# Optimization experiments

Measured on AMD Instinct MI355X. Metric: run time of the kernel, lower is better.

## Reference

```python
import jax, jax.numpy as jnp
import numpy as np

N_NODES = 50000
N_EDGES = 800000
F_IN = 128


def _sage_conv(x, src, dst, W_l, b_l, W_r, n_nodes):
    # PyG SAGEConv (mean aggr, normalize=False, root_weight=True):
    #   out_i = W_l @ mean_{j in N(i)} x_j + b_l + W_r @ x_i
    msg = x[src]  # [E, F] gather
    agg = jax.ops.segment_sum(msg, dst, num_segments=n_nodes)  # [N, F]
    cnt = jax.ops.segment_sum(jnp.ones((src.shape[0],), x.dtype), dst,
                              num_segments=n_nodes)  # [N]
    mean = agg / jnp.maximum(cnt, 1.0)[:, None]
    return mean @ W_l.T + b_l + x @ W_r.T


def setup_inputs() -> dict:
    key = jax.random.key(0)
    ks = jax.random.split(key, 16)
    inp = {}
    inp["x"] = jax.random.normal(ks[0], (N_NODES, F_IN), dtype=jnp.float32)
    inp["edge_index"] = jax.random.randint(ks[1], (2, N_EDGES), 0, N_NODES, dtype=jnp.int64)
    inp["reg_id"] = jax.random.randint(ks[2], (N_NODES,), 0, 22, dtype=jnp.int64)
    inp["dep_id"] = jax.random.randint(ks[3], (N_NODES,), 0, 96, dtype=jnp.int64)
    # learned parameters (kaiming-ish small random)
    inp["W_feat"] = jax.random.normal(ks[4], (32, F_IN), dtype=jnp.float32) * (1.0 / np.sqrt(F_IN))
    inp["b_feat"] = jnp.zeros((32,), dtype=jnp.float32)
    inp["reg_emb"] = jax.random.normal(ks[5], (22, 16), dtype=jnp.float32)
    inp["dep_emb"] = jax.random.normal(ks[6], (96, 16), dtype=jnp.float32)
    inp["W1_l"] = jax.random.normal(ks[7], (16, 64), dtype=jnp.float32) * 0.125
    inp["b1_l"] = jnp.zeros((16,), dtype=jnp.float32)
    inp["W1_r"] = jax.random.normal(ks[8], (16, 64), dtype=jnp.float32) * 0.125
    inp["W2_l"] = jax.random.normal(ks[9], (32, 16), dtype=jnp.float32) * 0.25
    inp["b2_l"] = jnp.zeros((32,), dtype=jnp.float32)
    inp["W2_r"] = jax.random.normal(ks[10], (32, 16), dtype=jnp.float32) * 0.25
    inp["W_lin"] = jax.random.normal(ks[11], (1, 32), dtype=jnp.float32) * 0.1767767
    inp["b_lin"] = jnp.zeros((1,), dtype=jnp.float32)
    return inp


def reference(x, edge_index, reg_id, dep_id, W_feat, b_feat, reg_emb, dep_emb,
              W1_l, b1_l, W1_r, W2_l, b2_l, W2_r, W_lin, b_lin):
    src, dst = edge_index[0], edge_index[1]
    reg_fm = reg_emb[reg_id]            # [N, 16]
    dep_fm = dep_emb[dep_id]            # [N, 16]
    h = x @ W_feat.T + b_feat           # [N, 32]
    h = jnp.concatenate([h, reg_fm, dep_fm], axis=1)  # [N, 64]
    h = jax.nn.relu(_sage_conv(h, src, dst, W1_l, b1_l, W1_r, N_NODES))  # [N, 16]
    h = jax.nn.relu(_sage_conv(h, src, dst, W2_l, b2_l, W2_r, N_NODES))  # [N, 32]
    return h @ W_lin.T + b_lin          # [N, 1]
```

## Files before the change

kernel.cpp:

```cpp
#include <hip/hip_runtime.h>

#define N_NODES 50000
#define N_EDGES 800000
#define HB 128
#define CHUNK (N_EDGES / HB)
#define CNTW ((N_NODES + 3) / 4)
#define NODE1_BLOCKS ((N_NODES + 63) / 64)
#define SCAN_BLK 256
#define SCAN_NBLK ((N_NODES + SCAN_BLK - 1) / SCAN_BLK)

__device__ __forceinline__ unsigned short f2bf(float f) {
    unsigned int b = __float_as_uint(f);
    b += 0x7fffu + ((b >> 16) & 1u);
    return (unsigned short)(b >> 16);
}

__global__ __launch_bounds__(256) void node1_hist_kernel(
    const float* __restrict__ x, const int* __restrict__ reg_id,
    const int* __restrict__ dep_id,
    const float* __restrict__ W_feat, const float* __restrict__ b_feat,
    const float* __restrict__ reg_emb, const float* __restrict__ dep_emb,
    const float* __restrict__ W1_l, const float* __restrict__ W1_r,
    const int* __restrict__ ei,
    unsigned short* __restrict__ p1bf, float* __restrict__ r1,
    unsigned int* __restrict__ part, unsigned char* __restrict__ lrank)
{
    __shared__ union U {
        struct N1 { float sx[64 * 132]; float sh[64 * 68]; } n1;
        unsigned int cnt[CNTW];
    } u;
    const int tid = threadIdx.x;

    if (blockIdx.x >= NODE1_BLOCKS) {
        const int g  = blockIdx.x - NODE1_BLOCKS;
        const int e0 = g * CHUNK;
        for (int i = tid; i < CNTW; i += 256) u.cnt[i] = 0u;
        __syncthreads();
        for (int i = tid; i < CHUNK; i += 256) {
            int d = ei[N_EDGES + e0 + i];
            unsigned sh_ = (unsigned)(d & 3) * 8u;
            unsigned old = atomicAdd(&u.cnt[d >> 2], 1u << sh_);
            lrank[e0 + i] = (unsigned char)((old >> sh_) & 0xffu);
        }
        __syncthreads();
        for (int i = tid; i < CNTW; i += 256)
            part[g * CNTW + i] = u.cnt[i];
        return;
    }

    const int node0 = blockIdx.x * 64;
    for (int i = tid; i < 64 * 32; i += 256) {
        int row = i >> 5, c4 = i & 31;
        float4 v = make_float4(0.f, 0.f, 0.f, 0.f);
        int n = node0 + row;
        if (n < N_NODES) v = *(const float4*)&x[n * 128 + c4 * 4];
        *(float4*)&u.n1.sx[row * 132 + c4 * 4] = v;
    }
    for (int i = tid; i < 64 * 16; i += 256) {
        int r = i >> 4, f = i & 15;
        int n = node0 + r;
        if (n < N_NODES) {
            u.n1.sh[r * 68 + 32 + f] = reg_emb[reg_id[n] * 16 + f];
            u.n1.sh[r * 68 + 48 + f] = dep_emb[dep_id[n] * 16 + f];
        }
    }
    __syncthreads();

    const int nl = tid & 63;
    const int j0 = __builtin_amdgcn_readfirstlane((tid >> 6) * 8);

    {
        float acc[8];
        #pragma unroll
        for (int jj = 0; jj < 8; ++jj) acc[jj] = b_feat[j0 + jj];
        #pragma unroll 4
        for (int k = 0; k < 128; k += 4) {
            float4 xv = *(const float4*)&u.n1.sx[nl * 132 + k];
            #pragma unroll
            for (int jj = 0; jj < 8; ++jj) {
                const float* wr = &W_feat[(j0 + jj) * 128 + k];
                acc[jj] += xv.x * wr[0] + xv.y * wr[1] + xv.z * wr[2] + xv.w * wr[3];
            }
        }
        #pragma unroll
        for (int jj = 0; jj < 8; ++jj) u.n1.sh[nl * 68 + j0 + jj] = acc[jj];
    }
    __syncthreads();

    {
        const float* Wbase = (j0 < 16) ? (W1_l + j0 * 64) : (W1_r + (j0 - 16) * 64);
        float acc[8];
        #pragma unroll
        for (int jj = 0; jj < 8; ++jj) acc[jj] = 0.f;
        #pragma unroll 4
        for (int k = 0; k < 64; k += 4) {
            float4 hv = *(const float4*)&u.n1.sh[nl * 68 + k];
            #pragma unroll
            for (int jj = 0; jj < 8; ++jj) {
                const float* wr = &Wbase[jj * 64 + k];
                acc[jj] += hv.x * wr[0] + hv.y * wr[1] + hv.z * wr[2] + hv.w * wr[3];
            }
        }
        int n = node0 + nl;
        if (n < N_NODES) {
            if (j0 < 16) {
                uint4 q;
                q.x = ((unsigned)f2bf(acc[1]) << 16) | f2bf(acc[0]);
                q.y = ((unsigned)f2bf(acc[3]) << 16) | f2bf(acc[2]);
                q.z = ((unsigned)f2bf(acc[5]) << 16) | f2bf(acc[4]);
                q.w = ((unsigned)f2bf(acc[7]) << 16) | f2bf(acc[6]);
                *(uint4*)&p1bf[n * 16 + j0] = q;
            } else {
                float* outp = r1 + n * 16 + (j0 - 16);
                *(float4*)outp       = make_float4(acc[0], acc[1], acc[2], acc[3]);
                *(float4*)(outp + 4) = make_float4(acc[4], acc[5], acc[6], acc[7]);
            }
        }
    }
}

__global__ __launch_bounds__(256) void bpscan_kernel(
    const unsigned int* __restrict__ part, unsigned char* __restrict__ bp,
    int* __restrict__ rowp1, int* __restrict__ parts)
{
    __shared__ int buf[2][256];
    int t = threadIdx.x;
    int n = blockIdx.x * 256 + t;
    int deg = 0;
    if (n < N_NODES) {
        int w = n >> 2;
        unsigned sh_ = (unsigned)(n & 3) * 8u;
        unsigned int loc[HB / 4];
        int s = 0;
        #pragma unroll
        for (int q = 0; q < HB / 4; ++q) {
            unsigned int wdat = 0;
            #pragma unroll
            for (int j = 0; j < 4; ++j) {
                wdat |= (unsigned)(s & 0xff) << (8 * j);
                s += (int)((part[(q * 4 + j) * CNTW + w] >> sh_) & 0xffu);
            }
            loc[q] = wdat;
        }
        deg = s;
        uint4* dst = (uint4*)&bp[(size_t)n * HB];
        const uint4* src = (const uint4*)loc;
        #pragma unroll
        for (int q = 0; q < HB / 16; ++q) dst[q] = src[q];
    }
    buf[0][t] = deg;
    __syncthreads();
    int cur = 0;
    for (int off = 1; off < 256; off <<= 1) {
        int nv = buf[cur][t] + ((t >= off) ? buf[cur][t - off] : 0);
        buf[cur ^ 1][t] = nv;
        cur ^= 1;
        __syncthreads();
    }
    int incl = buf[cur][t];
    if (n < N_NODES) rowp1[n] = incl - deg;
    if (t == 255) parts[blockIdx.x] = incl;
}

__global__ __launch_bounds__(256) void scanparts_kernel(
    const int* __restrict__ parts, int* __restrict__ poff)
{
    __shared__ int buf[2][256];
    int t = threadIdx.x;
    int pv = (t < SCAN_NBLK) ? parts[t] : 0;
    buf[0][t] = pv;
    __syncthreads();
    int cur = 0;
    for (int off = 1; off < 256; off <<= 1) {
        int nv = buf[cur][t] + ((t >= off) ? buf[cur][t - off] : 0);
        buf[cur ^ 1][t] = nv;
        cur ^= 1;
        __syncthreads();
    }
    if (t < SCAN_NBLK) poff[t] = buf[cur][t] - pv;
}

__global__ __launch_bounds__(256) void fill_kernel(
    const int* __restrict__ ei, const unsigned char* __restrict__ lrank,
    const int* __restrict__ rowp1, const int* __restrict__ poff,
    const unsigned char* __restrict__ bp, int* __restrict__ csrc)
{
    int t4 = (blockIdx.x * 256 + threadIdx.x) * 4;
    if (t4 >= N_EDGES) return;
    uint4 sv = *(const uint4*)&ei[t4];
    uint4 dv = *(const uint4*)&ei[N_EDGES + t4];
    unsigned lr4 = *(const unsigned*)&lrank[t4];

    #pragma unroll
    for (int j = 0; j < 4; ++j) {
        int d = (j == 0) ? (int)dv.x : (j == 1) ? (int)dv.y
              : (j == 2) ? (int)dv.z : (int)dv.w;
        int s = (j == 0) ? (int)sv.x : (j == 1) ? (int)sv.y
              : (j == 2) ? (int)sv.z : (int)sv.w;
        int g = (t4 + j) / CHUNK;
        int pos = rowp1[d] + poff[d >> 8] + (int)bp[(size_t)d * HB + g]
                + (int)((lr4 >> (8 * j)) & 0xffu);
        csrc[pos] = s;
    }
}

__global__ __launch_bounds__(256) void gather1_kernel(
    const int* __restrict__ rowp1, const int* __restrict__ poff,
    const int* __restrict__ csrc,
    const unsigned short* __restrict__ p1bf, const float* __restrict__ r1,
    const float* __restrict__ b1_l, unsigned short* __restrict__ h1bf)
{
    int n = (blockIdx.x * 256 + threadIdx.x) >> 6;
    int lane = threadIdx.x & 63;
    int slot = lane >> 2, f4 = lane & 3;
    int start = rowp1[n] + poff[n >> 8];
    int end = (n + 1 < N_NODES) ? rowp1[n + 1] + poff[(n + 1) >> 8] : N_EDGES;

    float4 acc = make_float4(0.f, 0.f, 0.f, 0.f);
    for (int eb = start; eb < end; eb += 16) {
        int e = eb + slot;
        if (e < end) {
            uint2 v = *(const uint2*)&p1bf[csrc[e] * 16 + f4 * 4];
            acc.x += __uint_as_float(v.x << 16);
            acc.y += __uint_as_float(v.x & 0xffff0000u);
            acc.z += __uint_as_float(v.y << 16);
            acc.w += __uint_as_float(v.y & 0xffff0000u);
        }
    }
    #pragma unroll
    for (int off = 4; off <= 32; off <<= 1) {
        acc.x += __shfl_xor(acc.x, off, 64);
        acc.y += __shfl_xor(acc.y, off, 64);
        acc.z += __shfl_xor(acc.z, off, 64);
        acc.w += __shfl_xor(acc.w, off, 64);
    }
    if (slot == 0) {
        float inv = 1.0f / fmaxf((float)(end - start), 1.0f);
        float4 rv = *(const float4*)&r1[n * 16 + f4 * 4];
        float4 bv = *(const float4*)&b1_l[f4 * 4];
        float ox = fmaxf(acc.x * inv + bv.x + rv.x, 0.f);
        float oy = fmaxf(acc.y * inv + bv.y + rv.y, 0.f);
        float oz = fmaxf(acc.z * inv + bv.z + rv.z, 0.f);
        float ow = fmaxf(acc.w * inv + bv.w + rv.w, 0.f);
        uint2 w;
        w.x = ((unsigned)f2bf(oy) << 16) | f2bf(ox);
        w.y = ((unsigned)f2bf(ow) << 16) | f2bf(oz);
        *(uint2*)&h1bf[n * 16 + f4 * 4] = w;
    }
}

__global__ __launch_bounds__(256) void gather2_kernel(
    const int* __restrict__ rowp1, const int* __restrict__ poff,
    const int* __restrict__ csrc, const unsigned short* __restrict__ h1bf,
    const float* __restrict__ W2_l, const float* __restrict__ b2_l,
    const float* __restrict__ W2_r, const float* __restrict__ W_lin,
    const float* __restrict__ b_lin, float* __restrict__ out)
{
    int n = (blockIdx.x * 256 + threadIdx.x) >> 6;
    int lane = threadIdx.x & 63;
    int slot = lane >> 2, f4 = lane & 3;
    int start = rowp1[n] + poff[n >> 8];
    int end = (n + 1 < N_NODES) ? rowp1[n + 1] + poff[(n + 1) >> 8] : N_EDGES;

    float4 acc = make_float4(0.f, 0.f, 0.f, 0.f);
    for (int eb = start; eb < end; eb += 16) {
        int e = eb + slot;
        if (e < end) {
            uint2 v = *(const uint2*)&h1bf[csrc[e] * 16 + f4 * 4];
            acc.x += __uint_as_float(v.x << 16);
            acc.y += __uint_as_float(v.x & 0xffff0000u);
            acc.z += __uint_as_float(v.y << 16);
            acc.w += __uint_as_float(v.y & 0xffff0000u);
        }
    }
    #pragma unroll
    for (int off = 4; off <= 32; off <<= 1) {
        acc.x += __shfl_xor(acc.x, off, 64);
        acc.y += __shfl_xor(acc.y, off, 64);
        acc.z += __shfl_xor(acc.z, off, 64);
        acc.w += __shfl_xor(acc.w, off, 64);
    }
    float inv = 1.0f / fmaxf((float)(end - start), 1.0f);
    float4 m2 = make_float4(acc.x * inv, acc.y * inv, acc.z * inv, acc.w * inv);
    uint2 hv = *(const uint2*)&h1bf[n * 16 + f4 * 4];
    float hn0 = __uint_as_float(hv.x << 16);
    float hn1 = __uint_as_float(hv.x & 0xffff0000u);
    float hn2 = __uint_as_float(hv.y << 16);
    float hn3 = __uint_as_float(hv.y & 0xffff0000u);

    int j0 = slot * 2;
    float4 wl0 = *(const float4*)&W2_l[j0 * 16 + f4 * 4];
    float4 wl1 = *(const float4*)&W2_l[(j0 + 1) * 16 + f4 * 4];
    float4 wr0 = *(const float4*)&W2_r[j0 * 16 + f4 * 4];
    float4 wr1 = *(const float4*)&W2_r[(j0 + 1) * 16 + f4 * 4];

    float pa = m2.x * wl0.x + m2.y * wl0.y + m2.z * wl0.z + m2.w * wl0.w
             + hn0 * wr0.x + hn1 * wr0.y + hn2 * wr0.z + hn3 * wr0.w;
    float pb = m2.x * wl1.x + m2.y * wl1.y + m2.z * wl1.z + m2.w * wl1.w
             + hn0 * wr1.x + hn1 * wr1.y + hn2 * wr1.z + hn3 * wr1.w;
    pa += __shfl_xor(pa, 1, 64); pa += __shfl_xor(pa, 2, 64);
    pb += __shfl_xor(pb, 1, 64); pb += __shfl_xor(pb, 2, 64);

    float h2a = fmaxf(pa + b2_l[j0], 0.f);
    float h2b = fmaxf(pb + b2_l[j0 + 1], 0.f);
    float w = h2a * W_lin[j0] + h2b * W_lin[j0 + 1];
    #pragma unroll
    for (int off = 4; off <= 32; off <<= 1) w += __shfl_xor(w, off, 64);
    if (lane == 0) out[n] = w + b_lin[0];
}

extern "C" void kernel_launch(void* const* d_in, const int* in_sizes, int n_in,
                              void* d_out, int out_size, void* d_ws, size_t ws_size,
                              hipStream_t stream) {
    const float* x       = (const float*)d_in[0];
    const int*   ei      = (const int*)  d_in[1];
    const int*   reg_id  = (const int*)  d_in[2];
    const int*   dep_id  = (const int*)  d_in[3];
    const float* W_feat  = (const float*)d_in[4];
    const float* b_feat  = (const float*)d_in[5];
    const float* reg_emb = (const float*)d_in[6];
    const float* dep_emb = (const float*)d_in[7];
    const float* W1_l    = (const float*)d_in[8];
    const float* b1_l    = (const float*)d_in[9];
    const float* W1_r    = (const float*)d_in[10];
    const float* W2_l    = (const float*)d_in[11];
    const float* b2_l    = (const float*)d_in[12];
    const float* W2_r    = (const float*)d_in[13];
    const float* W_lin   = (const float*)d_in[14];
    const float* b_lin   = (const float*)d_in[15];
    float* out = (float*)d_out;
    float* ws  = (float*)d_ws;

    const int N = N_NODES;
    float* r1 = ws;
    unsigned int* part = (unsigned int*)(ws + 16 * N);
    int* csrc  = (int*)(part + HB * CNTW);
    int* rowp1 = csrc + N_EDGES;
    int* parts = rowp1 + N;
    int* poff  = parts + 256;
    unsigned short* p1bf = (unsigned short*)(poff + 256);
    unsigned short* h1bf = p1bf + 16 * N;
    unsigned char* lrank = (unsigned char*)(h1bf + 16 * N);
    unsigned char* bp    = lrank + N_EDGES;

    node1_hist_kernel<<<NODE1_BLOCKS + HB, 256, 0, stream>>>(
        x, reg_id, dep_id, W_feat, b_feat, reg_emb, dep_emb, W1_l, W1_r,
        ei, p1bf, r1, part, lrank);

    bpscan_kernel<<<SCAN_NBLK, 256, 0, stream>>>(part, bp, rowp1, parts);

    scanparts_kernel<<<1, 256, 0, stream>>>(parts, poff);

    fill_kernel<<<(N_EDGES / 4 + 255) / 256, 256, 0, stream>>>(
        ei, lrank, rowp1, poff, bp, csrc);

    gather1_kernel<<<(N * 64) / 256, 256, 0, stream>>>(
        rowp1, poff, csrc, p1bf, r1, b1_l, h1bf);

    gather2_kernel<<<(N * 64) / 256, 256, 0, stream>>>(
        rowp1, poff, csrc, h1bf, W2_l, b2_l, W2_r, W_lin, b_lin, out);
}
```

Baseline: 104.7 us.

## Fuse bucket scan, partial-sum scan and CSR fill into one kernel with grid barrier

Merges the per-node prefix scan, the single-block scan of block partials, and the CSR fill into one kernel. The last block to finish, found through an atomic counter, scans the partials and sets a flag, and the other blocks spin on that flag before running a grid-strided fill. The control words are reset in the first kernel. This removes two kernel launches and their gaps. In exchange it relies on all 196 blocks being resident at once for the spin-wait, and the fill now runs on fewer threads that each loop over more edges.

```diff
diff --git a/kernel.cpp b/kernel.cpp
--- a/kernel.cpp
+++ b/kernel.cpp
@@ -23,13 +23,19 @@
     const float* __restrict__ W1_l, const float* __restrict__ W1_r,
     const int* __restrict__ ei,
     unsigned short* __restrict__ p1bf, float* __restrict__ r1,
-    unsigned int* __restrict__ part, unsigned char* __restrict__ lrank)
+    unsigned int* __restrict__ part, unsigned char* __restrict__ lrank,
+    int* __restrict__ ctrl)
 {
     __shared__ union U {
         struct N1 { float sx[64 * 132]; float sh[64 * 68]; } n1;
         unsigned int cnt[CNTW];
     } u;
     const int tid = threadIdx.x;
+
+    if (blockIdx.x == 0 && tid < 2) {
+        __hip_atomic_store(&ctrl[tid], 0, __ATOMIC_RELEASE,
+                           __HIP_MEMORY_SCOPE_AGENT);
+    }
 
     if (blockIdx.x >= NODE1_BLOCKS) {
         const int g  = blockIdx.x - NODE1_BLOCKS;
@@ -119,13 +125,19 @@
     }
 }
 
-__global__ __launch_bounds__(256) void bpscan_kernel(
-    const unsigned int* __restrict__ part, unsigned char* __restrict__ bp,
-    int* __restrict__ rowp1, int* __restrict__ parts)
+__global__ __launch_bounds__(256) void bpscan_fill_kernel(
+    const unsigned int* __restrict__ part, const int* __restrict__ ei,
+    const unsigned char* __restrict__ lrank,
+    unsigned char* __restrict__ bp, int* __restrict__ rowp1,
+    int* __restrict__ parts, int* __restrict__ poff,
+    int* __restrict__ ctrl, int* __restrict__ csrc)
 {
     __shared__ int buf[2][256];
-    int t = threadIdx.x;
-    int n = blockIdx.x * 256 + t;
+    __shared__ int sord;
+    const int t = threadIdx.x;
+    const int b = blockIdx.x;
+
+    int n = b * 256 + t;
     int deg = 0;
     if (n < N_NODES) {
         int w = n >> 2;
@@ -159,48 +171,58 @@
     }
     int incl = buf[cur][t];
     if (n < N_NODES) rowp1[n] = incl - deg;
-    if (t == 255) parts[blockIdx.x] = incl;
-}
-
-__global__ __launch_bounds__(256) void scanparts_kernel(
-    const int* __restrict__ parts, int* __restrict__ poff)
-{
-    __shared__ int buf[2][256];
-    int t = threadIdx.x;
-    int pv = (t < SCAN_NBLK) ? parts[t] : 0;
-    buf[0][t] = pv;
-    __syncthreads();
-    int cur = 0;
-    for (int off = 1; off < 256; off <<= 1) {
-        int nv = buf[cur][t] + ((t >= off) ? buf[cur][t - off] : 0);
-        buf[cur ^ 1][t] = nv;
-        cur ^= 1;
-        __syncthreads();
-    }
-    if (t < SCAN_NBLK) poff[t] = buf[cur][t] - pv;
-}
-
-__global__ __launch_bounds__(256) void fill_kernel(
-    const int* __restrict__ ei, const unsigned char* __restrict__ lrank,
-    const int* __restrict__ rowp1, const int* __restrict__ poff,
-    const unsigned char* __restrict__ bp, int* __restrict__ csrc)
-{
-    int t4 = (blockIdx.x * 256 + threadIdx.x) * 4;
-    if (t4 >= N_EDGES) return;
-    uint4 sv = *(const uint4*)&ei[t4];
-    uint4 dv = *(const uint4*)&ei[N_EDGES + t4];
-    unsigned lr4 = *(const unsigned*)&lrank[t4];
-
-    #pragma unroll
-    for (int j = 0; j < 4; ++j) {
-        int d = (j == 0) ? (int)dv.x : (j == 1) ? (int)dv.y
-              : (j == 2) ? (int)dv.z : (int)dv.w;
-        int s = (j == 0) ? (int)sv.x : (j == 1) ? (int)sv.y
-              : (j == 2) ? (int)sv.z : (int)sv.w;
-        int g = (t4 + j) / CHUNK;
-        int pos = rowp1[d] + poff[d >> 8] + (int)bp[(size_t)d * HB + g]
-                + (int)((lr4 >> (8 * j)) & 0xffu);
-        csrc[pos] = s;
+    if (t == 255) parts[b] = incl;
+
+    __threadfence();
+    __syncthreads();
+    if (t == 0)
+        sord = __hip_atomic_fetch_add(&ctrl[0], 1, __ATOMIC_ACQ_REL,
+                                      __HIP_MEMORY_SCOPE_AGENT);
+    __syncthreads();
+
+    if (sord == SCAN_NBLK - 1) {
+        __threadfence();
+        int pv = (t < SCAN_NBLK) ? parts[t] : 0;
+        buf[0][t] = pv;
+        __syncthreads();
+        cur = 0;
+        for (int off = 1; off < 256; off <<= 1) {
+            int nv = buf[cur][t] + ((t >= off) ? buf[cur][t - off] : 0);
+            buf[cur ^ 1][t] = nv;
+            cur ^= 1;
+            __syncthreads();
+        }
+        if (t < SCAN_NBLK) poff[t] = buf[cur][t] - pv;
+        __threadfence();
+        __syncthreads();
+        if (t == 0)
+            __hip_atomic_store(&ctrl[1], 1, __ATOMIC_RELEASE,
+                               __HIP_MEMORY_SCOPE_AGENT);
+    } else {
+        if (t == 0) {
+            while (__hip_atomic_load(&ctrl[1], __ATOMIC_ACQUIRE,
+                                     __HIP_MEMORY_SCOPE_AGENT) == 0)
+                __builtin_amdgcn_s_sleep(8);
+        }
+        __syncthreads();
+        __threadfence();
+    }
+
+    for (int t4 = (b * 256 + t) * 4; t4 < N_EDGES; t4 += SCAN_NBLK * 256 * 4) {
+        uint4 sv = *(const uint4*)&ei[t4];
+        uint4 dv = *(const uint4*)&ei[N_EDGES + t4];
+        unsigned lr4 = *(const unsigned*)&lrank[t4];
+        #pragma unroll
+        for (int j = 0; j < 4; ++j) {
+            int d = (j == 0) ? (int)dv.x : (j == 1) ? (int)dv.y
+                  : (j == 2) ? (int)dv.z : (int)dv.w;
+            int s = (j == 0) ? (int)sv.x : (j == 1) ? (int)sv.y
+                  : (j == 2) ? (int)sv.z : (int)sv.w;
+            int g = (t4 + j) / CHUNK;
+            int pos = rowp1[d] + poff[d >> 8] + (int)bp[(size_t)d * HB + g]
+                    + (int)((lr4 >> (8 * j)) & 0xffu);
+            csrc[pos] = s;
+        }
     }
 }
 
@@ -338,21 +360,18 @@
     int* rowp1 = csrc + N_EDGES;
     int* parts = rowp1 + N;
     int* poff  = parts + 256;
-    unsigned short* p1bf = (unsigned short*)(poff + 256);
+    int* ctrl  = poff + 256;
+    unsigned short* p1bf = (unsigned short*)(ctrl + 512);
     unsigned short* h1bf = p1bf + 16 * N;
     unsigned char* lrank = (unsigned char*)(h1bf + 16 * N);
     unsigned char* bp    = lrank + N_EDGES;
 
     node1_hist_kernel<<<NODE1_BLOCKS + HB, 256, 0, stream>>>(
         x, reg_id, dep_id, W_feat, b_feat, reg_emb, dep_emb, W1_l, W1_r,
-        ei, p1bf, r1, part, lrank);
-
-    bpscan_kernel<<<SCAN_NBLK, 256, 0, stream>>>(part, bp, rowp1, parts);
-
-    scanparts_kernel<<<1, 256, 0, stream>>>(parts, poff);
-
-    fill_kernel<<<(N_EDGES / 4 + 255) / 256, 256, 0, stream>>>(
-        ei, lrank, rowp1, poff, bp, csrc);
+        ei, p1bf, r1, part, lrank, ctrl);
+
+    bpscan_fill_kernel<<<SCAN_NBLK, 256, 0, stream>>>(
+        part, ei, lrank, bp, rowp1, parts, poff, ctrl, csrc);
 
     gather1_kernel<<<(N * 64) / 256, 256, 0, stream>>>(
         rowp1, poff, csrc, p1bf, r1, b1_l, h1bf);
```

New measurement: 163.0 us. 55.7% more time.
